# Kernel tuning notes

Hardware: AMD Instinct MI355X
Metric: run time of the kernel (lower is better)

## Reference

```python
import jax, jax.numpy as jnp
import numpy as np

B, S, D, F, E, R = 16, 1024, 1024, 4096, 8, 32
LORA_ALPHA = 16
SCALING = LORA_ALPHA / R  # 0.5


def setup_inputs() -> dict:
    key = jax.random.key(0)
    ks = jax.random.split(key, 16)
    sd = 0.02
    return {
        "x": jax.random.normal(ks[0], (B, S, D), jnp.float32),
        "router_w": jax.random.normal(ks[1], (E, D), jnp.float32) * sd,
        "router_b": jnp.zeros((E,), jnp.float32),
        "fc1_w": jax.random.normal(ks[2], (F, D), jnp.float32) * sd,
        "fc1_b": jnp.zeros((F,), jnp.float32),
        "fc2_w": jax.random.normal(ks[3], (D, F), jnp.float32) * sd,
        "fc2_b": jnp.zeros((D,), jnp.float32),
        "down_A_w": jax.random.normal(ks[4], (E, R, D), jnp.float32) * sd,
        "down_A_b": jnp.zeros((E, R), jnp.float32),
        "down_B_w": jax.random.normal(ks[5], (E, F, R), jnp.float32) * sd,
        "down_B_b": jnp.zeros((E, F), jnp.float32),
        "up_A_w": jax.random.normal(ks[6], (E, R, F), jnp.float32) * sd,
        "up_A_b": jnp.zeros((E, R), jnp.float32),
        "up_B_w": jax.random.normal(ks[7], (E, D, R), jnp.float32) * sd,
        "up_B_b": jnp.zeros((E, D), jnp.float32),
    }


def _lora_moe_sparse(inp, onehot, A_w, A_b, B_w, B_b):
    # inp: [b,t,c_in]; onehot: [b,t,E] hard top-1 dispatch mask
    # h: per-expert rank activations [b,t,E,R] (small: R=32)
    h = jnp.einsum('btc,erc->bter', inp, A_w) + A_b
    g = h * onehot[..., None]  # zero out non-selected experts (sparse dispatch)
    out = jnp.einsum('bter,eor->bto', g, B_w)
    out = out + jnp.einsum('bte,eo->bto', onehot, B_b)
    return out * SCALING


def reference(x, router_w, router_b, fc1_w, fc1_b, fc2_w, fc2_b,
              down_A_w, down_A_b, down_B_w, down_B_b,
              up_A_w, up_A_b, up_B_w, up_B_b):
    # router + top-1 hard routing (straight-through expert_choice)
    logits = jnp.einsum('btd,ed->bte', x, router_w) + router_b
    routing = jax.nn.softmax(logits, axis=-1)
    idx = jnp.argmax(routing, axis=-1)                       # [b,t]
    y_hard = jax.nn.one_hot(idx, E, dtype=x.dtype)           # [b,t,E]
    expert_choice = y_hard - jax.lax.stop_gradient(routing) + routing

    # down proj: frozen fc1 + sparse LoRA combine (dropout p=0.05 -> eval/identity)
    h1 = jnp.einsum('btd,fd->btf', x, fc1_w) + fc1_b
    h1 = h1 + _lora_moe_sparse(x, y_hard, down_A_w, down_A_b, down_B_w, down_B_b)
    a = jax.nn.gelu(h1, approximate=False)

    # up proj: frozen fc2 + sparse LoRA combine
    out = jnp.einsum('btf,df->btd', a, fc2_w) + fc2_b
    out = out + _lora_moe_sparse(a, y_hard, up_A_w, up_A_b, up_B_w, up_B_b)
    return out, (routing, expert_choice)
```

## Files before the change

kernel.cpp:

```cpp
#include <hip/hip_runtime.h>
#include <hip/hip_bf16.h>
#include <math.h>


#define M_TOK 16384
#define DIM_D 1024
#define DIM_F 4096
#define NEXP 8
#define RANK 32
#define NER 256
#define K1 1280
#define K2 4352

typedef __attribute__((ext_vector_type(8))) short bf16x8;
typedef __attribute__((ext_vector_type(4))) short sh4;
typedef __attribute__((ext_vector_type(4))) float f32x4;

__device__ inline short f2bs(float x) {
  __hip_bfloat16 h = __float2bfloat16(x);
  return *reinterpret_cast<short*>(&h);
}

__device__ inline void async16(const void* g, void* l) {
  __builtin_amdgcn_global_load_lds(
      (__attribute__((address_space(1))) void*)(g),
      (__attribute__((address_space(3))) void*)(l), 16, 0, 0);
}

__global__ __launch_bounds__(256) void convert_pitched(
    const float* __restrict__ in, short* __restrict__ out,
    int c8, int opitch, int n8)
{
  const int i = blockIdx.x * 256 + threadIdx.x;
  if (i >= n8) return;
  const int row = i / c8;
  const int c = (i % c8) * 8;
  const float4* p = (const float4*)(in + (size_t)row * (c8 * 8) + c);
  float4 u = p[0], v = p[1];
  bf16x8 r;
  r[0] = f2bs(u.x); r[1] = f2bs(u.y); r[2] = f2bs(u.z); r[3] = f2bs(u.w);
  r[4] = f2bs(v.x); r[5] = f2bs(v.y); r[6] = f2bs(v.z); r[7] = f2bs(v.w);
  *(bf16x8*)(out + (size_t)row * opitch + c) = r;
}

__global__ __launch_bounds__(256) void pack_lorab(
    const float* __restrict__ in, short* __restrict__ out,
    int Nn, int opitch, int ooff, int n8)
{
  const int i = blockIdx.x * 256 + threadIdx.x;
  if (i >= n8) return;
  const int e = i / (Nn * 4);
  const int rem = i % (Nn * 4);
  const int n = rem >> 2;
  const int r8 = (rem & 3) * 8;
  const float4* p = (const float4*)(in + ((size_t)e * Nn + n) * RANK + r8);
  float4 u = p[0], v = p[1];
  bf16x8 r;
  r[0] = f2bs(u.x); r[1] = f2bs(u.y); r[2] = f2bs(u.z); r[3] = f2bs(u.w);
  r[4] = f2bs(v.x); r[5] = f2bs(v.y); r[6] = f2bs(v.z); r[7] = f2bs(v.w);
  *(bf16x8*)(out + (size_t)n * opitch + ooff + e * RANK + r8) = r;
}

__global__ __launch_bounds__(256) void router_kernel(
    const float* __restrict__ X,
    const float* __restrict__ RW,
    const float* __restrict__ RB,
    float* __restrict__ routing_out,
    float* __restrict__ ec_out,
    int* __restrict__ idx_out,
    short* __restrict__ XB)
{
  const int wave = threadIdx.x >> 6;
  const int lane = threadIdx.x & 63;
  const int t = blockIdx.x * 4 + wave;

  const float4* xp = (const float4*)(X + (size_t)t * DIM_D);
  float4 xv[4];
#pragma unroll
  for (int i = 0; i < 4; ++i) xv[i] = xp[lane + 64 * i];

#pragma unroll
  for (int i = 0; i < 4; ++i) {
    sh4 o;
    o[0] = f2bs(xv[i].x); o[1] = f2bs(xv[i].y);
    o[2] = f2bs(xv[i].z); o[3] = f2bs(xv[i].w);
    *(sh4*)&XB[(size_t)t * K1 + (lane + 64 * i) * 4] = o;
  }

  float logit[NEXP];
#pragma unroll
  for (int e = 0; e < NEXP; ++e) {
    const float4* wp = (const float4*)(RW + (size_t)e * DIM_D);
    double p = 0.0;
#pragma unroll
    for (int i = 0; i < 4; ++i) {
      float4 w = wp[lane + 64 * i];
      p += (double)xv[i].x * w.x + (double)xv[i].y * w.y +
           (double)xv[i].z * w.z + (double)xv[i].w * w.w;
    }
#pragma unroll
    for (int off = 32; off > 0; off >>= 1) p += __shfl_xor(p, off);
    logit[e] = (float)p + RB[e];
  }
  float m = logit[0];
  int am = 0;
#pragma unroll
  for (int e = 1; e < NEXP; ++e)
    if (logit[e] > m) { m = logit[e]; am = e; }
  float pr[NEXP], s = 0.f;
#pragma unroll
  for (int e = 0; e < NEXP; ++e) { pr[e] = expf(logit[e] - m); s += pr[e]; }
  const float inv = 1.f / s;
  if (lane < NEXP) {
    float r = pr[lane] * inv;
    routing_out[(size_t)t * NEXP + lane] = r;
    float y = (lane == am) ? 1.f : 0.f;
    ec_out[(size_t)t * NEXP + lane] = (y - r) + r;
  }
  if (lane == 0) idx_out[t] = am;
}

template <int KM, int LDA, int OPITCH, int OOFF>
__global__ __launch_bounds__(256, 2) void lora_a_gemm(
    const short* __restrict__ A, const short* __restrict__ Bm,
    const float* __restrict__ bias, const int* __restrict__ idx,
    short* __restrict__ out)
{
  __shared__ __align__(16) short As[128 * 32];
  __shared__ __align__(16) short Bs[128 * 32];

  const int tid = threadIdx.x;
  const int m0 = blockIdx.y * 128;
  const int n0 = blockIdx.x * 128;
  const int lane = tid & 63;
  const int wv = tid >> 6;
  const int quad = lane >> 4;
  const int lrow = lane & 15;
  const int wr = wv >> 1;
  const int wc = wv & 1;
  const int r0 = tid >> 2;
  const int c4 = (tid & 3) * 8;

  f32x4 acc[4][4];
#pragma unroll
  for (int i = 0; i < 4; ++i)
#pragma unroll
    for (int j = 0; j < 4; ++j) acc[i][j] = (f32x4){0.f, 0.f, 0.f, 0.f};

  for (int it = 0; it < KM / 32; ++it) {
    const int k = it * 32;
    const short* a0 = A + (size_t)(m0 + r0) * LDA + k + c4;
    const short* b0 = Bm + (size_t)(n0 + r0) * KM + k + c4;
    async16(a0, &As[tid * 8]);
    async16(a0 + (size_t)64 * LDA, &As[2048 + tid * 8]);
    async16(b0, &Bs[tid * 8]);
    async16(b0 + (size_t)64 * KM, &Bs[2048 + tid * 8]);
    __syncthreads();

    bf16x8 af[4], bfv[4];
#pragma unroll
    for (int i = 0; i < 4; ++i)
      af[i] = *(const bf16x8*)&As[(wr * 64 + i * 16 + lrow) * 32 + quad * 8];
#pragma unroll
    for (int j = 0; j < 4; ++j)
      bfv[j] = *(const bf16x8*)&Bs[(wc * 64 + j * 16 + lrow) * 32 + quad * 8];
#pragma unroll
    for (int i = 0; i < 4; ++i)
#pragma unroll
      for (int j = 0; j < 4; ++j)
        acc[i][j] = __builtin_amdgcn_mfma_f32_16x16x32_bf16(af[i], bfv[j],
                                                            acc[i][j], 0, 0, 0);
    __syncthreads();
  }

  float cb[4];
#pragma unroll
  for (int j = 0; j < 4; ++j) cb[j] = bias[n0 + wc * 64 + j * 16 + lrow];

#pragma unroll
  for (int i = 0; i < 4; ++i) {
#pragma unroll
    for (int reg = 0; reg < 4; ++reg) {
      const int t = m0 + wr * 64 + i * 16 + quad * 4 + reg;
      const int e = idx[t];
#pragma unroll
      for (int j = 0; j < 4; ++j) {
        const int gc = n0 + wc * 64 + j * 16 + lrow;
        float v = ((gc >> 5) == e) ? 0.5f * (acc[i][j][reg] + cb[j]) : 0.f;
        out[(size_t)t * OPITCH + OOFF + gc] = f2bs(v);
      }
    }
  }
}

template <int K, int N, int POUT, int EPI>
__global__ __launch_bounds__(512, 2) void gemm256(
    const short* __restrict__ A, const short* __restrict__ Bm,
    const float* __restrict__ LB, const float* __restrict__ bias,
    const int* __restrict__ idx, void* __restrict__ outv)
{
  static_assert(K % 128 == 0, "K must be multiple of 128");
  __shared__ __align__(16) short lds[65536];

  const int tid = threadIdx.x;
  const int lane = tid & 63;
  const int wv = tid >> 6;
  const int wr = wv >> 2;
  const int wc = wv & 3;
  const int quad = lane >> 4;
  const int lrow = lane & 15;

  const int gx = gridDim.x;
  int id = blockIdx.y * gx + blockIdx.x;
  const int nwg = gx * gridDim.y;
  id = (id & 7) * (nwg >> 3) + (id >> 3);
  const int m0 = (id / gx) * 256;
  const int n0 = (id % gx) * 256;

  const int srow = wv * 32 + (lane >> 2);
  const int scol = ((lane & 3) * 8) ^ ((lane >= 32) ? 16 : 0);
  const short* Asrc = A + (size_t)(m0 + srow) * K + scol;
  const short* Bsrc = Bm + (size_t)(n0 + srow) * K + scol;
  const int sdst = wv * 1024 + lane * 8;

  const int innerA = (lrow * 32 + quad * 8) ^ ((lrow & 8) ? 16 : 0);
  const int aoff = wr * 4096 + innerA;
  const int boff = 16384 + wc * 2048 + innerA;

  f32x4 acc[8][4];
#pragma unroll
  for (int i = 0; i < 8; ++i)
#pragma unroll
    for (int j = 0; j < 4; ++j) acc[i][j] = (f32x4){0.f, 0.f, 0.f, 0.f};

  bf16x8 af[4], bfv[4];

#define STG(src, t, h, tens, buf)                                              \
  {                                                                            \
    _Pragma("unroll") for (int jj = 0; jj < 2; ++jj)                           \
        async16((src) + (size_t)(jj * 16) * K + (t) * 64 + (h) * 32,           \
                &lds[(buf) * 32768 + (tens) + (h) * 8192 + sdst + jj * 512]);  \
  }
#define RDB(ks, buf)                                                           \
  _Pragma("unroll") for (int j = 0; j < 4; ++j)                                \
      bfv[j] = *(const bf16x8*)&lds[(buf) * 32768 + (ks) * 8192 + boff + j * 512];
#define RDA(mh, ks, buf)                                                       \
  _Pragma("unroll") for (int i = 0; i < 4; ++i)                                \
      af[i] = *(const bf16x8*)&lds[(buf) * 32768 + (ks) * 8192 + aoff +        \
                                   ((mh) * 4 + i) * 512];
#define MM(mh)                                                                 \
  {                                                                            \
    __builtin_amdgcn_s_setprio(1);                                             \
    _Pragma("unroll") for (int i = 0; i < 4; ++i)                              \
    _Pragma("unroll") for (int j = 0; j < 4; ++j)                              \
        acc[(mh) * 4 + i][j] = __builtin_amdgcn_mfma_f32_16x16x32_bf16(        \
            af[i], bfv[j], acc[(mh) * 4 + i][j], 0, 0, 0);                     \
    __builtin_amdgcn_s_setprio(0);                                             \
  }
#define BARR asm volatile("s_barrier" ::: "memory")
#define WV4 asm volatile("s_waitcnt vmcnt(4)" ::: "memory")
#define WV0 asm volatile("s_waitcnt vmcnt(0)" ::: "memory")

  STG(Asrc, 0, 0, 0, 0);
  STG(Bsrc, 0, 0, 16384, 0);
  STG(Asrc, 0, 1, 0, 0);
  STG(Bsrc, 0, 1, 16384, 0);
  WV4; BARR;

  constexpr int nIter = K / 128;
  for (int it = 0; it < nIter - 1; ++it) {
    const int t1 = 2 * it + 1, t2 = 2 * it + 2;
    RDB(0, 0); RDA(0, 0, 0); STG(Asrc, t1, 0, 0, 1);     BARR; MM(0);      BARR;
    RDA(1, 0, 0);            STG(Bsrc, t1, 0, 16384, 1); BARR; MM(1); WV4; BARR;
    RDB(1, 0); RDA(0, 1, 0); STG(Asrc, t1, 1, 0, 1);     BARR; MM(0);      BARR;
    RDA(1, 1, 0);            STG(Bsrc, t1, 1, 16384, 1); BARR; MM(1); WV4; BARR;
    RDB(0, 1); RDA(0, 0, 1); STG(Asrc, t2, 0, 0, 0);     BARR; MM(0);      BARR;
    RDA(1, 0, 1);            STG(Bsrc, t2, 0, 16384, 0); BARR; MM(1); WV4; BARR;
    RDB(1, 1); RDA(0, 1, 1); STG(Asrc, t2, 1, 0, 0);     BARR; MM(0);      BARR;
    RDA(1, 1, 1);            STG(Bsrc, t2, 1, 16384, 0); BARR; MM(1); WV4; BARR;
  }
  {
    const int t1 = 2 * nIter - 1;
    RDB(0, 0); RDA(0, 0, 0); STG(Asrc, t1, 0, 0, 1);     BARR; MM(0);      BARR;
    RDA(1, 0, 0);            STG(Bsrc, t1, 0, 16384, 1); BARR; MM(1); WV4; BARR;
    RDB(1, 0); RDA(0, 1, 0); STG(Asrc, t1, 1, 0, 1);     BARR; MM(0);      BARR;
    RDA(1, 1, 0);            STG(Bsrc, t1, 1, 16384, 1); BARR; MM(1); WV4; BARR;
    RDB(0, 1); RDA(0, 0, 1);                             BARR; MM(0);      BARR;
    RDA(1, 0, 1);                                        BARR; MM(1); WV0; BARR;
    RDB(1, 1); RDA(0, 1, 1);                             BARR; MM(0);      BARR;
    RDA(1, 1, 1);                                        BARR; MM(1);
  }
#undef STG
#undef RDB
#undef RDA
#undef MM
#undef BARR
#undef WV4
#undef WV0

  const int orow0 = m0 + wr * 128;
  const int ocol0 = n0 + wc * 64;
  float cb[4];
#pragma unroll
  for (int j = 0; j < 4; ++j) cb[j] = bias[ocol0 + j * 16 + lrow];

#pragma unroll
  for (int i = 0; i < 8; ++i) {
#pragma unroll
    for (int reg = 0; reg < 4; ++reg) {
      const int t = orow0 + i * 16 + quad * 4 + reg;
      const int e = idx[t];
      const float* lbp = LB + (size_t)e * N;
#pragma unroll
      for (int j = 0; j < 4; ++j) {
        const int gc = ocol0 + j * 16 + lrow;
        float v = acc[i][j][reg] + cb[j] + 0.5f * lbp[gc];
        if (EPI == 1) {
          v = 0.5f * v * (1.0f + erff(v * 0.70710678118654752f));
          ((short*)outv)[(size_t)t * POUT + gc] = f2bs(v);
        } else {
          ((float*)outv)[(size_t)t * POUT + gc] = v;
        }
      }
    }
  }
}

extern "C" void kernel_launch(void* const* d_in, const int* in_sizes, int n_in,
                              void* d_out, int out_size, void* d_ws, size_t ws_size,
                              hipStream_t stream) {
  (void)in_sizes; (void)n_in; (void)out_size; (void)ws_size;
  const float* x        = (const float*)d_in[0];
  const float* router_w = (const float*)d_in[1];
  const float* router_b = (const float*)d_in[2];
  const float* fc1_w    = (const float*)d_in[3];
  const float* fc1_b    = (const float*)d_in[4];
  const float* fc2_w    = (const float*)d_in[5];
  const float* fc2_b    = (const float*)d_in[6];
  const float* down_A_w = (const float*)d_in[7];
  const float* down_A_b = (const float*)d_in[8];
  const float* down_B_w = (const float*)d_in[9];
  const float* down_B_b = (const float*)d_in[10];
  const float* up_A_w   = (const float*)d_in[11];
  const float* up_A_b   = (const float*)d_in[12];
  const float* up_B_w   = (const float*)d_in[13];
  const float* up_B_b   = (const float*)d_in[14];

  char* ws = (char*)d_ws;
  size_t off = 0;
  int* idxp  = (int*)ws;              off += (size_t)M_TOK * 4;
  short* xbw = (short*)(ws + off);    off += (size_t)M_TOK * K1 * 2;
  short* aw  = (short*)(ws + off);    off += (size_t)M_TOK * K2 * 2;
  short* B1w = (short*)(ws + off);    off += (size_t)DIM_F * K1 * 2;
  short* B2w = (short*)(ws + off);    off += (size_t)DIM_D * K2 * 2;
  short* dAb = (short*)(ws + off);    off += (size_t)NER * DIM_D * 2;
  short* uAb = (short*)(ws + off);    off += (size_t)NER * DIM_F * 2;

  float* out = (float*)d_out;
  float* routing = out + (size_t)M_TOK * DIM_D;
  float* ec = routing + (size_t)M_TOK * NEXP;

  convert_pitched<<<2048, 256, 0, stream>>>(fc1_w, B1w, 128, K1, 524288);
  convert_pitched<<<2048, 256, 0, stream>>>(fc2_w, B2w, 512, K2, 524288);
  convert_pitched<<<128,  256, 0, stream>>>(down_A_w, dAb, 128, DIM_D, 32768);
  convert_pitched<<<512,  256, 0, stream>>>(up_A_w,   uAb, 512, DIM_F, 131072);
  pack_lorab<<<512, 256, 0, stream>>>(down_B_w, B1w, DIM_F, K1, DIM_D, 131072);
  pack_lorab<<<128, 256, 0, stream>>>(up_B_w,   B2w, DIM_D, K2, DIM_F, 32768);

  router_kernel<<<M_TOK / 4, 256, 0, stream>>>(x, router_w, router_b, routing,
                                               ec, idxp, xbw);
  lora_a_gemm<DIM_D, K1, K1, DIM_D>
      <<<dim3(2, M_TOK / 128), 256, 0, stream>>>(xbw, dAb, down_A_b, idxp, xbw);
  gemm256<K1, DIM_F, K2, 1>
      <<<dim3(DIM_F / 256, M_TOK / 256), 512, 0, stream>>>(
          xbw, B1w, down_B_b, fc1_b, idxp, aw);
  lora_a_gemm<DIM_F, K2, K2, DIM_F>
      <<<dim3(2, M_TOK / 128), 256, 0, stream>>>(aw, uAb, up_A_b, idxp, aw);
  gemm256<K2, DIM_D, DIM_D, 0>
      <<<dim3(DIM_D / 256, M_TOK / 256), 512, 0, stream>>>(
          aw, B2w, up_B_b, fc2_b, idxp, out);
}
```

Before: 678.5 us.

## Pre-pack GEMM operands into swizzled 256x32 blocks for contiguous async loads

Every bf16 operand (activations, weights, LoRA A/B, intermediate GELU output) is now written into a blocked layout: 256-row by 32-column tiles stored contiguously, with an XOR swizzle pre-applied. The GEMM kernels can then issue fully contiguous 16-byte global-to-LDS loads per tile, with no strided row addressing, and LDS reads match the swizzle directly. The gemm256 main loop is also restructured into a TILE macro that prefetches the next tile earlier, with a vmcnt(8) wait. The cost is scattered writes in the producer epilogues and converters, and a layout that only fits these fixed dimensions.

```diff
diff --git a/kernel.cpp b/kernel.cpp
--- a/kernel.cpp
+++ b/kernel.cpp
@@ -27,25 +27,32 @@
       (__attribute__((address_space(3))) void*)(l), 16, 0, 0);
 }
 
-__global__ __launch_bounds__(256) void convert_pitched(
+__device__ inline size_t pk_blk(int row, int k, int KP) {
+  return (size_t)(row >> 8) * (KP >> 5) + (k >> 5);
+}
+__device__ inline int pk_off(int row, int k) {
+  return (row & 255) * 32 + ((k & 31) ^ ((row & 8) << 1));
+}
+
+__global__ __launch_bounds__(256) void convert_packed(
     const float* __restrict__ in, short* __restrict__ out,
-    int c8, int opitch, int n8)
+    int c8, int KP, int n8)
 {
   const int i = blockIdx.x * 256 + threadIdx.x;
   if (i >= n8) return;
   const int row = i / c8;
-  const int c = (i % c8) * 8;
-  const float4* p = (const float4*)(in + (size_t)row * (c8 * 8) + c);
+  const int k = (i % c8) * 8;
+  const float4* p = (const float4*)(in + (size_t)row * (c8 * 8) + k);
   float4 u = p[0], v = p[1];
   bf16x8 r;
   r[0] = f2bs(u.x); r[1] = f2bs(u.y); r[2] = f2bs(u.z); r[3] = f2bs(u.w);
   r[4] = f2bs(v.x); r[5] = f2bs(v.y); r[6] = f2bs(v.z); r[7] = f2bs(v.w);
-  *(bf16x8*)(out + (size_t)row * opitch + c) = r;
+  *(bf16x8*)(out + pk_blk(row, k, KP) * 8192 + pk_off(row, k)) = r;
 }
 
 __global__ __launch_bounds__(256) void pack_lorab(
     const float* __restrict__ in, short* __restrict__ out,
-    int Nn, int opitch, int ooff, int n8)
+    int Nn, int KP, int ooff, int n8)
 {
   const int i = blockIdx.x * 256 + threadIdx.x;
   if (i >= n8) return;
@@ -53,12 +60,13 @@
   const int rem = i % (Nn * 4);
   const int n = rem >> 2;
   const int r8 = (rem & 3) * 8;
+  const int k = ooff + e * RANK + r8;
   const float4* p = (const float4*)(in + ((size_t)e * Nn + n) * RANK + r8);
   float4 u = p[0], v = p[1];
   bf16x8 r;
   r[0] = f2bs(u.x); r[1] = f2bs(u.y); r[2] = f2bs(u.z); r[3] = f2bs(u.w);
   r[4] = f2bs(v.x); r[5] = f2bs(v.y); r[6] = f2bs(v.z); r[7] = f2bs(v.w);
-  *(bf16x8*)(out + (size_t)n * opitch + ooff + e * RANK + r8) = r;
+  *(bf16x8*)(out + pk_blk(n, k, KP) * 8192 + pk_off(n, k)) = r;
 }
 
 __global__ __launch_bounds__(256) void router_kernel(
@@ -84,7 +92,8 @@
     sh4 o;
     o[0] = f2bs(xv[i].x); o[1] = f2bs(xv[i].y);
     o[2] = f2bs(xv[i].z); o[3] = f2bs(xv[i].w);
-    *(sh4*)&XB[(size_t)t * K1 + (lane + 64 * i) * 4] = o;
+    const int k0 = (lane + 64 * i) * 4;
+    *(sh4*)&XB[pk_blk(t, k0, K1) * 8192 + pk_off(t, k0)] = o;
   }
 
   float logit[NEXP];
@@ -120,7 +129,7 @@
   if (lane == 0) idx_out[t] = am;
 }
 
-template <int KM, int LDA, int OPITCH, int OOFF>
+template <int KM, int LDA, int OPK, int OOFF>
 __global__ __launch_bounds__(256, 2) void lora_a_gemm(
     const short* __restrict__ A, const short* __restrict__ Bm,
     const float* __restrict__ bias, const int* __restrict__ idx,
@@ -138,8 +147,7 @@
   const int lrow = lane & 15;
   const int wr = wv >> 1;
   const int wc = wv & 1;
-  const int r0 = tid >> 2;
-  const int c4 = (tid & 3) * 8;
+  const int swz = (quad * 8) ^ ((lrow & 8) << 1);
 
   f32x4 acc[4][4];
 #pragma unroll
@@ -147,23 +155,27 @@
 #pragma unroll
     for (int j = 0; j < 4; ++j) acc[i][j] = (f32x4){0.f, 0.f, 0.f, 0.f};
 
+  const short* Ab = A + ((size_t)(m0 >> 8) * (LDA >> 5)) * 8192 +
+                    (size_t)(m0 & 255) * 32;
+  const short* Bb = Bm + ((size_t)(n0 >> 8) * (KM >> 5)) * 8192 +
+                    (size_t)(n0 & 255) * 32;
+
   for (int it = 0; it < KM / 32; ++it) {
-    const int k = it * 32;
-    const short* a0 = A + (size_t)(m0 + r0) * LDA + k + c4;
-    const short* b0 = Bm + (size_t)(n0 + r0) * KM + k + c4;
+    const short* a0 = Ab + (size_t)it * 8192 + tid * 8;
+    const short* b0 = Bb + (size_t)it * 8192 + tid * 8;
     async16(a0, &As[tid * 8]);
-    async16(a0 + (size_t)64 * LDA, &As[2048 + tid * 8]);
+    async16(a0 + 2048, &As[tid * 8 + 2048]);
     async16(b0, &Bs[tid * 8]);
-    async16(b0 + (size_t)64 * KM, &Bs[2048 + tid * 8]);
+    async16(b0 + 2048, &Bs[tid * 8 + 2048]);
     __syncthreads();
 
     bf16x8 af[4], bfv[4];
 #pragma unroll
     for (int i = 0; i < 4; ++i)
-      af[i] = *(const bf16x8*)&As[(wr * 64 + i * 16 + lrow) * 32 + quad * 8];
+      af[i] = *(const bf16x8*)&As[(wr * 64 + i * 16 + lrow) * 32 + swz];
 #pragma unroll
     for (int j = 0; j < 4; ++j)
-      bfv[j] = *(const bf16x8*)&Bs[(wc * 64 + j * 16 + lrow) * 32 + quad * 8];
+      bfv[j] = *(const bf16x8*)&Bs[(wc * 64 + j * 16 + lrow) * 32 + swz];
 #pragma unroll
     for (int i = 0; i < 4; ++i)
 #pragma unroll
@@ -187,7 +199,8 @@
       for (int j = 0; j < 4; ++j) {
         const int gc = n0 + wc * 64 + j * 16 + lrow;
         float v = ((gc >> 5) == e) ? 0.5f * (acc[i][j][reg] + cb[j]) : 0.f;
-        out[(size_t)t * OPITCH + OOFF + gc] = f2bs(v);
+        const int k = OOFF + gc;
+        out[pk_blk(t, k, OPK) * 8192 + pk_off(t, k)] = f2bs(v);
       }
     }
   }
@@ -217,15 +230,12 @@
   const int m0 = (id / gx) * 256;
   const int n0 = (id % gx) * 256;
 
-  const int srow = wv * 32 + (lane >> 2);
-  const int scol = ((lane & 3) * 8) ^ ((lane >= 32) ? 16 : 0);
-  const short* Asrc = A + (size_t)(m0 + srow) * K + scol;
-  const short* Bsrc = Bm + (size_t)(n0 + srow) * K + scol;
-  const int sdst = wv * 1024 + lane * 8;
-
-  const int innerA = (lrow * 32 + quad * 8) ^ ((lrow & 8) ? 16 : 0);
-  const int aoff = wr * 4096 + innerA;
-  const int boff = 16384 + wc * 2048 + innerA;
+  const short* Abase = A + (size_t)(m0 >> 8) * (K >> 5) * 8192;
+  const short* Bbase = Bm + (size_t)(n0 >> 8) * (K >> 5) * 8192;
+
+  const int swz = (quad * 8) ^ ((lrow & 8) << 1);
+  const int arowb = wr * 4096 + lrow * 32 + swz;
+  const int browb = 16384 + wc * 2048 + lrow * 32 + swz;
 
   f32x4 acc[8][4];
 #pragma unroll
@@ -235,68 +245,71 @@
 
   bf16x8 af[4], bfv[4];
 
-#define STG(src, t, h, tens, buf)                                              \
-  {                                                                            \
-    _Pragma("unroll") for (int jj = 0; jj < 2; ++jj)                           \
-        async16((src) + (size_t)(jj * 16) * K + (t) * 64 + (h) * 32,           \
-                &lds[(buf) * 32768 + (tens) + (h) * 8192 + sdst + jj * 512]);  \
-  }
-#define RDB(ks, buf)                                                           \
-  _Pragma("unroll") for (int j = 0; j < 4; ++j)                                \
-      bfv[j] = *(const bf16x8*)&lds[(buf) * 32768 + (ks) * 8192 + boff + j * 512];
-#define RDA(mh, ks, buf)                                                       \
-  _Pragma("unroll") for (int i = 0; i < 4; ++i)                                \
-      af[i] = *(const bf16x8*)&lds[(buf) * 32768 + (ks) * 8192 + aoff +        \
-                                   ((mh) * 4 + i) * 512];
-#define MM(mh)                                                                 \
-  {                                                                            \
-    __builtin_amdgcn_s_setprio(1);                                             \
-    _Pragma("unroll") for (int i = 0; i < 4; ++i)                              \
-    _Pragma("unroll") for (int j = 0; j < 4; ++j)                              \
-        acc[(mh) * 4 + i][j] = __builtin_amdgcn_mfma_f32_16x16x32_bf16(        \
-            af[i], bfv[j], acc[(mh) * 4 + i][j], 0, 0, 0);                     \
-    __builtin_amdgcn_s_setprio(0);                                             \
-  }
-#define BARR asm volatile("s_barrier" ::: "memory")
+#define STG(base, t, h, tens, buf)                                            \
+  {                                                                           \
+    const short* s_ = (base) + (size_t)(2 * (t) + (h)) * 8192 + tid * 8;      \
+    short* d_ = &lds[(buf)*32768 + (tens) + (h)*8192 + tid * 8];              \
+    async16(s_, d_);                                                          \
+    async16(s_ + 4096, d_ + 4096);                                            \
+  }
+#define RDB(h, buf)                                                           \
+  _Pragma("unroll") for (int j = 0; j < 4; ++j)                               \
+      bfv[j] = *(const bf16x8*)&lds[(buf)*32768 + (h)*8192 + browb + j * 512];
+#define RDA(mh, h, buf)                                                       \
+  _Pragma("unroll") for (int i = 0; i < 4; ++i)                               \
+      af[i] = *(const bf16x8*)&lds[(buf)*32768 + (h)*8192 + arowb +           \
+                                   (mh)*2048 + i * 512];
+#define MM(mh)                                                                \
+  {                                                                           \
+    __builtin_amdgcn_s_setprio(1);                                            \
+    _Pragma("unroll") for (int i = 0; i < 4; ++i)                             \
+    _Pragma("unroll") for (int j = 0; j < 4; ++j)                             \
+        acc[(mh)*4 + i][j] = __builtin_amdgcn_mfma_f32_16x16x32_bf16(         \
+            af[i], bfv[j], acc[(mh)*4 + i][j], 0, 0, 0);                      \
+    __builtin_amdgcn_s_setprio(0);                                            \
+  }
+#define BARR __builtin_amdgcn_s_barrier()
+#define WV8 asm volatile("s_waitcnt vmcnt(8)" ::: "memory")
 #define WV4 asm volatile("s_waitcnt vmcnt(4)" ::: "memory")
 #define WV0 asm volatile("s_waitcnt vmcnt(0)" ::: "memory")
-
-  STG(Asrc, 0, 0, 0, 0);
-  STG(Bsrc, 0, 0, 16384, 0);
-  STG(Asrc, 0, 1, 0, 0);
-  STG(Bsrc, 0, 1, 16384, 0);
+#define TILE(t, b, nb)                                                        \
+  STG(Abase, (t) + 1, 0, 0, nb);                                              \
+  STG(Bbase, (t) + 1, 0, 16384, nb);                                          \
+  RDB(0, b); RDA(0, 0, b); BARR; MM(0); BARR;                                 \
+  STG(Abase, (t) + 1, 1, 0, nb);                                              \
+  STG(Bbase, (t) + 1, 1, 16384, nb);                                          \
+  RDA(1, 0, b); BARR; MM(1); WV8; BARR;                                       \
+  RDB(1, b); RDA(0, 1, b); BARR; MM(0); BARR;                                 \
+  RDA(1, 1, b); BARR; MM(1); WV4; BARR;
+
+  STG(Abase, 0, 0, 0, 0);
+  STG(Bbase, 0, 0, 16384, 0);
+  STG(Abase, 0, 1, 0, 0);
+  STG(Bbase, 0, 1, 16384, 0);
   WV4; BARR;
 
-  constexpr int nIter = K / 128;
-  for (int it = 0; it < nIter - 1; ++it) {
-    const int t1 = 2 * it + 1, t2 = 2 * it + 2;
-    RDB(0, 0); RDA(0, 0, 0); STG(Asrc, t1, 0, 0, 1);     BARR; MM(0);      BARR;
-    RDA(1, 0, 0);            STG(Bsrc, t1, 0, 16384, 1); BARR; MM(1); WV4; BARR;
-    RDB(1, 0); RDA(0, 1, 0); STG(Asrc, t1, 1, 0, 1);     BARR; MM(0);      BARR;
-    RDA(1, 1, 0);            STG(Bsrc, t1, 1, 16384, 1); BARR; MM(1); WV4; BARR;
-    RDB(0, 1); RDA(0, 0, 1); STG(Asrc, t2, 0, 0, 0);     BARR; MM(0);      BARR;
-    RDA(1, 0, 1);            STG(Bsrc, t2, 0, 16384, 0); BARR; MM(1); WV4; BARR;
-    RDB(1, 1); RDA(0, 1, 1); STG(Asrc, t2, 1, 0, 0);     BARR; MM(0);      BARR;
-    RDA(1, 1, 1);            STG(Bsrc, t2, 1, 16384, 0); BARR; MM(1); WV4; BARR;
-  }
+  constexpr int NT = K / 64;
+  for (int p = 0; p < NT / 2 - 1; ++p) {
+    const int t0 = 2 * p;
+    TILE(t0, 0, 1);
+    TILE(t0 + 1, 1, 0);
+  }
+  TILE(NT - 2, 0, 1);
   {
-    const int t1 = 2 * nIter - 1;
-    RDB(0, 0); RDA(0, 0, 0); STG(Asrc, t1, 0, 0, 1);     BARR; MM(0);      BARR;
-    RDA(1, 0, 0);            STG(Bsrc, t1, 0, 16384, 1); BARR; MM(1); WV4; BARR;
-    RDB(1, 0); RDA(0, 1, 0); STG(Asrc, t1, 1, 0, 1);     BARR; MM(0);      BARR;
-    RDA(1, 1, 0);            STG(Bsrc, t1, 1, 16384, 1); BARR; MM(1); WV4; BARR;
-    RDB(0, 1); RDA(0, 0, 1);                             BARR; MM(0);      BARR;
-    RDA(1, 0, 1);                                        BARR; MM(1); WV0; BARR;
-    RDB(1, 1); RDA(0, 1, 1);                             BARR; MM(0);      BARR;
-    RDA(1, 1, 1);                                        BARR; MM(1);
+    RDB(0, 1); RDA(0, 0, 1); BARR; MM(0); BARR;
+    RDA(1, 0, 1);            BARR; MM(1); WV0; BARR;
+    RDB(1, 1); RDA(0, 1, 1); BARR; MM(0); BARR;
+    RDA(1, 1, 1);                  MM(1);
   }
 #undef STG
 #undef RDB
 #undef RDA
 #undef MM
 #undef BARR
+#undef WV8
 #undef WV4
 #undef WV0
+#undef TILE
 
   const int orow0 = m0 + wr * 128;
   const int ocol0 = n0 + wc * 64;
@@ -317,7 +330,7 @@
         float v = acc[i][j][reg] + cb[j] + 0.5f * lbp[gc];
         if (EPI == 1) {
           v = 0.5f * v * (1.0f + erff(v * 0.70710678118654752f));
-          ((short*)outv)[(size_t)t * POUT + gc] = f2bs(v);
+          ((short*)outv)[pk_blk(t, gc, POUT) * 8192 + pk_off(t, gc)] = f2bs(v);
         } else {
           ((float*)outv)[(size_t)t * POUT + gc] = v;
         }
@@ -360,10 +373,10 @@
   float* routing = out + (size_t)M_TOK * DIM_D;
   float* ec = routing + (size_t)M_TOK * NEXP;
 
-  convert_pitched<<<2048, 256, 0, stream>>>(fc1_w, B1w, 128, K1, 524288);
-  convert_pitched<<<2048, 256, 0, stream>>>(fc2_w, B2w, 512, K2, 524288);
-  convert_pitched<<<128,  256, 0, stream>>>(down_A_w, dAb, 128, DIM_D, 32768);
-  convert_pitched<<<512,  256, 0, stream>>>(up_A_w,   uAb, 512, DIM_F, 131072);
+  convert_packed<<<2048, 256, 0, stream>>>(fc1_w, B1w, 128, K1, 524288);
+  convert_packed<<<2048, 256, 0, stream>>>(fc2_w, B2w, 512, K2, 524288);
+  convert_packed<<<128,  256, 0, stream>>>(down_A_w, dAb, 128, DIM_D, 32768);
+  convert_packed<<<512,  256, 0, stream>>>(up_A_w,   uAb, 512, DIM_F, 131072);
   pack_lorab<<<512, 256, 0, stream>>>(down_B_w, B1w, DIM_F, K1, DIM_D, 131072);
   pack_lorab<<<128, 256, 0, stream>>>(up_B_w,   B2w, DIM_D, K2, DIM_F, 32768);
 
```

Result: slower. 764.3 us (+12.6%).
